# Kernel tuning notes

Measured on AMD Instinct MI355X. Metric: run time of the kernel, lower is better.

## Reference

```python
import jax, jax.numpy as jnp
import numpy as np


def setup_inputs() -> dict:
    key = jax.random.key(0)
    k1, k2 = jax.random.split(key)
    B, C, H, W = 8, 128, 96, 160
    x1 = jax.random.normal(k1, (B, C, H, W), dtype=jnp.float32)
    x2 = jax.random.normal(k2, (B, C, H, W), dtype=jnp.float32)
    return {"x1": x1, "x2": x2, "d": 4}


def reference(x1, x2, d):
    # x1, x2: (B, C, H, W); output: (B, (2d+1)^2, H, W)
    b, c, h, w = x1.shape
    x2p = jnp.pad(x2, ((0, 0), (0, 0), (d, d), (d, d)))
    # Loop over the small fixed (2d+1)^2 displacement set (81 for d=4);
    # each term is a channel-reduced elementwise product (shift-multiply-sum).
    corrs = [
        jnp.einsum("bchw,bchw->bhw", x1,
                   jax.lax.dynamic_slice(x2p, (0, 0, i, j), (b, c, h, w)))
        for i in range(2 * d + 1)
        for j in range(2 * d + 1)
    ]
    out = jnp.stack(corrs, axis=1)  # (B, (2d+1)^2, H, W)
    return out / c
```

## Files before the change

kernel.cpp:

```cpp
#include <hip/hip_runtime.h>
#include <hip/hip_bf16.h>
#include <stdint.h>

#define Bb 8
#define Cc 128
#define Hh 96
#define Ww 160
#define HW (Hh*Ww)
#define Kk 81

typedef __attribute__((ext_vector_type(8))) short short8;
typedef __attribute__((ext_vector_type(4))) float floatx4;
typedef __attribute__((ext_vector_type(4))) unsigned int uintx4;

__device__ __forceinline__ uint32_t bf16rne(float f) {
  uint32_t u = __float_as_uint(f);
  return (u + 0x7FFFu + ((u >> 16) & 1u)) >> 16;
}


__global__ __launch_bounds__(512, 2)
void corr_kernel(const float* __restrict__ x1, const float* __restrict__ x2,
                 float* __restrict__ out) {
  __shared__ __align__(16) ushort ldsX2[16*24*40];
  __shared__ __align__(16) ushort ldsX1[8*16*40];

  const int tid = threadIdx.x;
  const int w0 = blockIdx.x * 16;
  const int h0 = blockIdx.y * 8;
  const int b  = blockIdx.z;

  const int lane = tid & 63;
  const int wv   = tid >> 6;
  const int vy = wv & 3, vx = wv >> 2;
  const int n = lane & 15, quad = lane >> 4;
  const int s = n >> 3, pw = n & 7;

  floatx4 acc[10];
#pragma unroll
  for (int t = 0; t < 10; ++t) acc[t] = (floatx4){0.f, 0.f, 0.f, 0.f};

  for (int ck = 0; ck < 4; ++ck) {
    const int c0 = ck * 32;
    if (ck) __syncthreads();

#pragma unroll
    for (int it = 0; it < 3; ++it) {
      int T   = it * 512 + tid;
      int w24 = T % 24;
      int t2  = T / 24;
      int rw  = t2 & 15;
      int cg  = t2 >> 4;
      int gh = h0 - 4 + rw;
      int gw = w0 - 4 + w24;
      bool ok = ((unsigned)gh < Hh) && ((unsigned)gw < Ww);
      const float* src = x2 + ((size_t)(b*Cc + c0 + cg*8) * HW + gh*Ww + gw);
      uint32_t p0, p1, p2, p3;
      {
        float a0 = ok ? src[0*HW] : 0.f;
        float a1 = ok ? src[1*HW] : 0.f;
        float a2 = ok ? src[2*HW] : 0.f;
        float a3 = ok ? src[3*HW] : 0.f;
        float a4 = ok ? src[4*HW] : 0.f;
        float a5 = ok ? src[5*HW] : 0.f;
        float a6 = ok ? src[6*HW] : 0.f;
        float a7 = ok ? src[7*HW] : 0.f;
        p0 = bf16rne(a0) | (bf16rne(a1) << 16);
        p1 = bf16rne(a2) | (bf16rne(a3) << 16);
        p2 = bf16rne(a4) | (bf16rne(a5) << 16);
        p3 = bf16rne(a6) | (bf16rne(a7) << 16);
      }
      *(uintx4*)&ldsX2[(rw*24 + w24)*40 + cg*8] = (uintx4){p0, p1, p2, p3};
    }

    {
      int T  = tid;
      int wl = T & 15;
      int t2 = T >> 4;
      int rl = t2 & 7;
      int cg = t2 >> 3;
      const float* src = x1 + ((size_t)(b*Cc + c0 + cg*8) * HW
                               + (h0 + rl)*Ww + (w0 + wl));
      uint32_t p0, p1, p2, p3;
      float a0 = src[0*HW], a1 = src[1*HW], a2 = src[2*HW], a3 = src[3*HW];
      float a4 = src[4*HW], a5 = src[5*HW], a6 = src[6*HW], a7 = src[7*HW];
      p0 = bf16rne(a0) | (bf16rne(a1) << 16);
      p1 = bf16rne(a2) | (bf16rne(a3) << 16);
      p2 = bf16rne(a4) | (bf16rne(a5) << 16);
      p3 = bf16rne(a6) | (bf16rne(a7) << 16);
      *(uintx4*)&ldsX1[(rl*16 + wl)*40 + cg*8] = (uintx4){p0, p1, p2, p3};
    }

    __syncthreads();

    short8 bfrag = *(const short8*)&ldsX1[((2*vy + s)*16 + 8*vx + pw)*40 + quad*8];
#pragma unroll
    for (int t = 0; t < 10; ++t) {
      short8 afrag = *(const short8*)&ldsX2[((2*vy + t)*24 + 8*vx + n)*40 + quad*8];
      acc[t] = __builtin_amdgcn_mfma_f32_16x16x32_bf16(afrag, bfrag, acc[t], 0, 0, 0);
    }
  }

  const float scale = 1.0f / 128.0f;
  const int ph  = h0 + 2*vy + s;
  const int pwg = w0 + 8*vx + pw;
#pragma unroll
  for (int t = 0; t < 10; ++t) {
    int di = t - 4 - s;
    if ((unsigned)(di + 4) > 8u) continue;
#pragma unroll
    for (int r = 0; r < 4; ++r) {
      int dj = quad*4 + r - 4 - pw;
      if ((unsigned)(dj + 4) > 8u) continue;
      int kk = (di + 4) * 9 + (dj + 4);
      out[((size_t)b*Kk + kk) * HW + ph*Ww + pwg] = acc[t][r] * scale;
    }
  }
}

extern "C" void kernel_launch(void* const* d_in, const int* in_sizes, int n_in,
                              void* d_out, int out_size, void* d_ws, size_t ws_size,
                              hipStream_t stream) {
  const float* x1 = (const float*)d_in[0];
  const float* x2 = (const float*)d_in[1];
  float* out = (float*)d_out;
  dim3 grid(Ww/16, Hh/8, Bb);
  corr_kernel<<<grid, dim3(512, 1, 1), 0, stream>>>(x1, x2, out);
}
```

Measured before the change: 202.1 us.

## Prefetch next channel chunk into registers during MFMA and use nontemporal stores

Loads each channel chunk's global data into registers one iteration ahead, so the next chunk's loads are in flight while MFMAs run on the current LDS tile. Address computation is hoisted out of the loop, with clamped addresses so loads are unconditional and masking is applied after the load. The output writes use nontemporal stores, and launch bounds request 4 blocks per CU. The cost is more live registers (32 prefetch floats), which may conflict with the higher occupancy hint and cause spills.

Measured after the change: 304.1 us. 50.5% more time.

```diff
diff --git a/kernel.cpp b/kernel.cpp
--- a/kernel.cpp
+++ b/kernel.cpp
@@ -19,7 +19,7 @@
 }
 
 
-__global__ __launch_bounds__(512, 2)
+__global__ __launch_bounds__(512, 4)
 void corr_kernel(const float* __restrict__ x1, const float* __restrict__ x2,
                  float* __restrict__ out) {
   __shared__ __align__(16) ushort ldsX2[16*24*40];
@@ -36,67 +36,88 @@
   const int n = lane & 15, quad = lane >> 4;
   const int s = n >> 3, pw = n & 7;
 
+  const float* srcX2[3]; bool okX2[3]; int dstX2[3];
+#pragma unroll
+  for (int it = 0; it < 3; ++it) {
+    int T   = it * 512 + tid;
+    int w24 = T % 24;
+    int t2  = T / 24;
+    int rw  = t2 & 15;
+    int cg  = t2 >> 4;
+    int gh = h0 - 4 + rw;
+    int gw = w0 - 4 + w24;
+    bool ok = ((unsigned)gh < Hh) && ((unsigned)gw < Ww);
+    int ghc = min(max(gh, 0), Hh - 1);
+    int gwc = min(max(gw, 0), Ww - 1);
+    srcX2[it] = x2 + ((size_t)(b*Cc + cg*8) * HW + ghc*Ww + gwc);
+    okX2[it]  = ok;
+    dstX2[it] = (rw*24 + w24)*40 + cg*8;
+  }
+  const float* srcX1; int dstX1;
+  {
+    int wl = tid & 15;
+    int t2 = tid >> 4;
+    int rl = t2 & 7;
+    int cg = t2 >> 3;
+    srcX1 = x1 + ((size_t)(b*Cc + cg*8) * HW + (h0 + rl)*Ww + (w0 + wl));
+    dstX1 = (rl*16 + wl)*40 + cg*8;
+  }
+
+  const ushort* bsrc = &ldsX1[((2*vy + s)*16 + 8*vx + pw)*40 + quad*8];
+  const ushort* asrc0 = &ldsX2[(2*vy)*24*40 + (8*vx + n)*40 + quad*8];
+
   floatx4 acc[10];
 #pragma unroll
   for (int t = 0; t < 10; ++t) acc[t] = (floatx4){0.f, 0.f, 0.f, 0.f};
 
+  float r2[3][8], r1[8];
+
+#pragma unroll
+  for (int it = 0; it < 3; ++it)
+#pragma unroll
+    for (int k = 0; k < 8; ++k) r2[it][k] = srcX2[it][k*HW];
+#pragma unroll
+  for (int k = 0; k < 8; ++k) r1[k] = srcX1[k*HW];
+
+#pragma unroll
   for (int ck = 0; ck < 4; ++ck) {
-    const int c0 = ck * 32;
     if (ck) __syncthreads();
 
 #pragma unroll
     for (int it = 0; it < 3; ++it) {
-      int T   = it * 512 + tid;
-      int w24 = T % 24;
-      int t2  = T / 24;
-      int rw  = t2 & 15;
-      int cg  = t2 >> 4;
-      int gh = h0 - 4 + rw;
-      int gw = w0 - 4 + w24;
-      bool ok = ((unsigned)gh < Hh) && ((unsigned)gw < Ww);
-      const float* src = x2 + ((size_t)(b*Cc + c0 + cg*8) * HW + gh*Ww + gw);
-      uint32_t p0, p1, p2, p3;
-      {
-        float a0 = ok ? src[0*HW] : 0.f;
-        float a1 = ok ? src[1*HW] : 0.f;
-        float a2 = ok ? src[2*HW] : 0.f;
-        float a3 = ok ? src[3*HW] : 0.f;
-        float a4 = ok ? src[4*HW] : 0.f;
-        float a5 = ok ? src[5*HW] : 0.f;
-        float a6 = ok ? src[6*HW] : 0.f;
-        float a7 = ok ? src[7*HW] : 0.f;
-        p0 = bf16rne(a0) | (bf16rne(a1) << 16);
-        p1 = bf16rne(a2) | (bf16rne(a3) << 16);
-        p2 = bf16rne(a4) | (bf16rne(a5) << 16);
-        p3 = bf16rne(a6) | (bf16rne(a7) << 16);
+      uint32_t p[4];
+#pragma unroll
+      for (int j = 0; j < 4; ++j) {
+        float a = okX2[it] ? r2[it][2*j]   : 0.f;
+        float bb= okX2[it] ? r2[it][2*j+1] : 0.f;
+        p[j] = bf16rne(a) | (bf16rne(bb) << 16);
       }
-      *(uintx4*)&ldsX2[(rw*24 + w24)*40 + cg*8] = (uintx4){p0, p1, p2, p3};
+      *(uintx4*)&ldsX2[dstX2[it]] = (uintx4){p[0], p[1], p[2], p[3]};
     }
-
     {
-      int T  = tid;
-      int wl = T & 15;
-      int t2 = T >> 4;
-      int rl = t2 & 7;
-      int cg = t2 >> 3;
-      const float* src = x1 + ((size_t)(b*Cc + c0 + cg*8) * HW
-                               + (h0 + rl)*Ww + (w0 + wl));
-      uint32_t p0, p1, p2, p3;
-      float a0 = src[0*HW], a1 = src[1*HW], a2 = src[2*HW], a3 = src[3*HW];
-      float a4 = src[4*HW], a5 = src[5*HW], a6 = src[6*HW], a7 = src[7*HW];
-      p0 = bf16rne(a0) | (bf16rne(a1) << 16);
-      p1 = bf16rne(a2) | (bf16rne(a3) << 16);
-      p2 = bf16rne(a4) | (bf16rne(a5) << 16);
-      p3 = bf16rne(a6) | (bf16rne(a7) << 16);
-      *(uintx4*)&ldsX1[(rl*16 + wl)*40 + cg*8] = (uintx4){p0, p1, p2, p3};
+      uint32_t p[4];
+#pragma unroll
+      for (int j = 0; j < 4; ++j)
+        p[j] = bf16rne(r1[2*j]) | (bf16rne(r1[2*j+1]) << 16);
+      *(uintx4*)&ldsX1[dstX1] = (uintx4){p[0], p[1], p[2], p[3]};
     }
 
     __syncthreads();
 
-    short8 bfrag = *(const short8*)&ldsX1[((2*vy + s)*16 + 8*vx + pw)*40 + quad*8];
+    if (ck < 3) {
+      const int co = (ck + 1) * 32;
+#pragma unroll
+      for (int it = 0; it < 3; ++it)
+#pragma unroll
+        for (int k = 0; k < 8; ++k) r2[it][k] = srcX2[it][(co + k)*HW];
+#pragma unroll
+      for (int k = 0; k < 8; ++k) r1[k] = srcX1[(co + k)*HW];
+    }
+
+    short8 bfrag = *(const short8*)bsrc;
 #pragma unroll
     for (int t = 0; t < 10; ++t) {
-      short8 afrag = *(const short8*)&ldsX2[((2*vy + t)*24 + 8*vx + n)*40 + quad*8];
+      short8 afrag = *(const short8*)(asrc0 + t*24*40);
       acc[t] = __builtin_amdgcn_mfma_f32_16x16x32_bf16(afrag, bfrag, acc[t], 0, 0, 0);
     }
   }
@@ -113,7 +134,8 @@
       int dj = quad*4 + r - 4 - pw;
       if ((unsigned)(dj + 4) > 8u) continue;
       int kk = (di + 4) * 9 + (dj + 4);
-      out[((size_t)b*Kk + kk) * HW + ph*Ww + pwg] = acc[t][r] * scale;
+      __builtin_nontemporal_store(acc[t][r] * scale,
+          &out[((size_t)b*Kk + kk) * HW + ph*Ww + pwg]);
     }
   }
 }
```

## Widen tile to 32 columns per block to cut x2 halo reloads

Applied to the files above, without the earlier changes.

Each block now covers 8x32 output pixels instead of 8x16. Every wave computes two 8-column sub-tiles with two accumulator sets, which shrinks the fraction of x2 halo columns loaded per block (40 columns staged for 32 outputs instead of 24 for 16). The launch-bounds occupancy hint also rises from 2 to 4 blocks per CU. Register pressure doubles for accumulators, LDS per block grows, and the grid halves to 5x12x8 blocks, which may underfill the GPU.

Result: slower. 213.3 us (+5.6%).

```diff
diff --git a/kernel.cpp b/kernel.cpp
--- a/kernel.cpp
+++ b/kernel.cpp
@@ -19,40 +19,42 @@
 }
 
 
-__global__ __launch_bounds__(512, 2)
+__global__ __launch_bounds__(512, 4)
 void corr_kernel(const float* __restrict__ x1, const float* __restrict__ x2,
                  float* __restrict__ out) {
-  __shared__ __align__(16) ushort ldsX2[16*24*40];
-  __shared__ __align__(16) ushort ldsX1[8*16*40];
+  __shared__ __align__(16) ushort ldsX2[16*40*40];
+  __shared__ __align__(16) ushort ldsX1[8*32*40];
 
   const int tid = threadIdx.x;
-  const int w0 = blockIdx.x * 16;
+  const int w0 = blockIdx.x * 32;
   const int h0 = blockIdx.y * 8;
   const int b  = blockIdx.z;
 
   const int lane = tid & 63;
   const int wv   = tid >> 6;
-  const int vy = wv & 3, vx = wv >> 2;
+  const int vy = wv & 3, g = wv >> 2;
   const int n = lane & 15, quad = lane >> 4;
-  const int s = n >> 3, pw = n & 7;
+  const int s = n >> 3, pwl = n & 7;
 
-  floatx4 acc[10];
+  floatx4 acc[2][10];
 #pragma unroll
-  for (int t = 0; t < 10; ++t) acc[t] = (floatx4){0.f, 0.f, 0.f, 0.f};
+  for (int u = 0; u < 2; ++u)
+#pragma unroll
+    for (int t = 0; t < 10; ++t) acc[u][t] = (floatx4){0.f, 0.f, 0.f, 0.f};
 
   for (int ck = 0; ck < 4; ++ck) {
     const int c0 = ck * 32;
     if (ck) __syncthreads();
 
 #pragma unroll
-    for (int it = 0; it < 3; ++it) {
+    for (int it = 0; it < 5; ++it) {
       int T   = it * 512 + tid;
-      int w24 = T % 24;
-      int t2  = T / 24;
+      int w40 = T % 40;
+      int t2  = T / 40;
       int rw  = t2 & 15;
       int cg  = t2 >> 4;
       int gh = h0 - 4 + rw;
-      int gw = w0 - 4 + w24;
+      int gw = w0 - 4 + w40;
       bool ok = ((unsigned)gh < Hh) && ((unsigned)gw < Ww);
       const float* src = x2 + ((size_t)(b*Cc + c0 + cg*8) * HW + gh*Ww + gw);
       uint32_t p0, p1, p2, p3;
@@ -70,13 +72,14 @@
         p2 = bf16rne(a4) | (bf16rne(a5) << 16);
         p3 = bf16rne(a6) | (bf16rne(a7) << 16);
       }
-      *(uintx4*)&ldsX2[(rw*24 + w24)*40 + cg*8] = (uintx4){p0, p1, p2, p3};
+      *(uintx4*)&ldsX2[(rw*40 + w40)*40 + cg*8] = (uintx4){p0, p1, p2, p3};
     }
 
-    {
-      int T  = tid;
-      int wl = T & 15;
-      int t2 = T >> 4;
+#pragma unroll
+    for (int it = 0; it < 2; ++it) {
+      int T  = it * 512 + tid;
+      int wl = T & 31;
+      int t2 = T >> 5;
       int rl = t2 & 7;
       int cg = t2 >> 3;
       const float* src = x1 + ((size_t)(b*Cc + c0 + cg*8) * HW
@@ -88,32 +91,38 @@
       p1 = bf16rne(a2) | (bf16rne(a3) << 16);
       p2 = bf16rne(a4) | (bf16rne(a5) << 16);
       p3 = bf16rne(a6) | (bf16rne(a7) << 16);
-      *(uintx4*)&ldsX1[(rl*16 + wl)*40 + cg*8] = (uintx4){p0, p1, p2, p3};
+      *(uintx4*)&ldsX1[(rl*32 + wl)*40 + cg*8] = (uintx4){p0, p1, p2, p3};
     }
 
     __syncthreads();
 
-    short8 bfrag = *(const short8*)&ldsX1[((2*vy + s)*16 + 8*vx + pw)*40 + quad*8];
 #pragma unroll
-    for (int t = 0; t < 10; ++t) {
-      short8 afrag = *(const short8*)&ldsX2[((2*vy + t)*24 + 8*vx + n)*40 + quad*8];
-      acc[t] = __builtin_amdgcn_mfma_f32_16x16x32_bf16(afrag, bfrag, acc[t], 0, 0, 0);
+    for (int u = 0; u < 2; ++u) {
+      short8 bfrag = *(const short8*)&ldsX1[((2*vy + s)*32 + 16*g + 8*u + pwl)*40 + quad*8];
+#pragma unroll
+      for (int t = 0; t < 10; ++t) {
+        short8 afrag = *(const short8*)&ldsX2[((2*vy + t)*40 + 16*g + 8*u + n)*40 + quad*8];
+        acc[u][t] = __builtin_amdgcn_mfma_f32_16x16x32_bf16(afrag, bfrag, acc[u][t], 0, 0, 0);
+      }
     }
   }
 
   const float scale = 1.0f / 128.0f;
-  const int ph  = h0 + 2*vy + s;
-  const int pwg = w0 + 8*vx + pw;
+  const int ph = h0 + 2*vy + s;
 #pragma unroll
-  for (int t = 0; t < 10; ++t) {
-    int di = t - 4 - s;
-    if ((unsigned)(di + 4) > 8u) continue;
+  for (int u = 0; u < 2; ++u) {
+    const int pwg = w0 + 16*g + 8*u + pwl;
 #pragma unroll
-    for (int r = 0; r < 4; ++r) {
-      int dj = quad*4 + r - 4 - pw;
-      if ((unsigned)(dj + 4) > 8u) continue;
-      int kk = (di + 4) * 9 + (dj + 4);
-      out[((size_t)b*Kk + kk) * HW + ph*Ww + pwg] = acc[t][r] * scale;
+    for (int t = 0; t < 10; ++t) {
+      int di = t - 4 - s;
+      if ((unsigned)(di + 4) > 8u) continue;
+#pragma unroll
+      for (int r = 0; r < 4; ++r) {
+        int dj = quad*4 + r - 4 - pwl;
+        if ((unsigned)(dj + 4) > 8u) continue;
+        int kk = (di + 4) * 9 + (dj + 4);
+        out[((size_t)b*Kk + kk) * HW + ph*Ww + pwg] = acc[u][t][r] * scale;
+      }
     }
   }
 }
@@ -124,6 +133,6 @@
   const float* x1 = (const float*)d_in[0];
   const float* x2 = (const float*)d_in[1];
   float* out = (float*)d_out;
-  dim3 grid(Ww/16, Hh/8, Bb);
+  dim3 grid(Ww/32, Hh/8, Bb);
   corr_kernel<<<grid, dim3(512, 1, 1), 0, stream>>>(x1, x2, out);
 }
```
